# Kernel tuning notes

Hardware: AMD Instinct MI355X
Metric: run time of the kernel (lower is better)

The kernel has to match this reference:

```python
import jax, jax.numpy as jnp
import numpy as np

N_NODES = 100000
N_EDGES = 3200000
D_IN = 128
D_OUT = 128


def setup_inputs() -> dict:
    key = jax.random.key(0)
    kx, kw, kb, kr, kc, kv = jax.random.split(key, 6)
    x = jax.random.normal(kx, (N_NODES, D_IN), dtype=jnp.float32)
    W = jax.random.normal(kw, (D_OUT, D_IN), dtype=jnp.float32) * (1.0 / np.sqrt(D_IN))
    b = jax.random.normal(kb, (D_OUT,), dtype=jnp.float32) * 0.01
    adj_rows = jax.random.randint(kr, (N_EDGES,), 0, N_NODES, dtype=jnp.int32)
    adj_cols = jax.random.randint(kc, (N_EDGES,), 0, N_NODES, dtype=jnp.int32)
    adj_vals = jax.random.uniform(kv, (N_EDGES,), dtype=jnp.float32)
    return {"x": x, "W": W, "b": b, "adj_rows": adj_rows,
            "adj_cols": adj_cols, "adj_vals": adj_vals}


def reference(x, W, b, adj_rows, adj_cols, adj_vals):
    # linear: out = x @ W.T + b   -> [N, D_OUT]
    out = jnp.einsum('ni,oi->no', x, W) + b
    # spmm(adj, out): row r = sum over edges (r, c, v) of v * out[c]
    gathered = out[adj_cols] * adj_vals[:, None]          # [E, D_OUT]
    agg = jax.ops.segment_sum(gathered, adj_rows, num_segments=x.shape[0])
    return jax.nn.elu(agg)
```

## Files before the change

### kernel.cpp

```cpp
#include <hip/hip_runtime.h>
#include <hip/hip_bf16.h>
#include <cmath>

#define RPB      32
#define FB_CAP   1280
#define SB_SHIFT 11
#define NSB_MAX  64
#define TILE     2048
#define CH_PER_SB 34

typedef __attribute__((ext_vector_type(8))) short short8;
typedef __attribute__((ext_vector_type(4))) float floatx4;

__device__ __forceinline__ unsigned short f2bf(float f) {
    unsigned int u = __float_as_uint(f);
    u += 0x7FFFu + ((u >> 16) & 1u);
    return (unsigned short)(u >> 16);
}

__global__ __launch_bounds__(256) void gemm_mfma_kernel(
    const float* __restrict__ x, const float* __restrict__ W,
    const float* __restrict__ b, unsigned short* __restrict__ Yb, int N)
{
    __shared__ unsigned short Wb[128][136];
    __shared__ unsigned short Xb[64][136];
    const int t    = threadIdx.x;
    const int wave = t >> 6;
    const int lane = t & 63;
    const int col  = lane & 15;
    const int quad = lane >> 4;
    const int rowbase = blockIdx.x * 64;

#pragma unroll
    for (int i = 0; i < 16; ++i) {
        const int idx = t + 256 * i;
        const int o = idx >> 5, k4 = (idx & 31) * 4;
        const float4 v = *(const float4*)&W[(size_t)idx * 4];
        Wb[o][k4 + 0] = f2bf(v.x); Wb[o][k4 + 1] = f2bf(v.y);
        Wb[o][k4 + 2] = f2bf(v.z); Wb[o][k4 + 3] = f2bf(v.w);
    }
#pragma unroll
    for (int i = 0; i < 8; ++i) {
        const int idx = t + 256 * i;
        const int row = idx >> 5, k4 = (idx & 31) * 4;
        const int gr = rowbase + row;
        float4 v = make_float4(0.f, 0.f, 0.f, 0.f);
        if (gr < N) v = *(const float4*)&x[(size_t)gr * 128 + k4];
        Xb[row][k4 + 0] = f2bf(v.x); Xb[row][k4 + 1] = f2bf(v.y);
        Xb[row][k4 + 2] = f2bf(v.z); Xb[row][k4 + 3] = f2bf(v.w);
    }
    __syncthreads();

    float bias[8];
#pragma unroll
    for (int nt = 0; nt < 8; ++nt) bias[nt] = b[nt * 16 + col];

    floatx4 acc[8] = {};
    const int mrow = wave * 16;
#pragma unroll
    for (int k0 = 0; k0 < 128; k0 += 32) {
        const short8 a = *(const short8*)&Xb[mrow + col][k0 + quad * 8];
#pragma unroll
        for (int nt = 0; nt < 8; ++nt) {
            const short8 bf = *(const short8*)&Wb[nt * 16 + col][k0 + quad * 8];
            acc[nt] = __builtin_amdgcn_mfma_f32_16x16x32_bf16(a, bf, acc[nt], 0, 0, 0);
        }
    }
#pragma unroll
    for (int nt = 0; nt < 8; ++nt) {
#pragma unroll
        for (int reg = 0; reg < 4; ++reg) {
            const int gr = rowbase + mrow + quad * 4 + reg;
            if (gr < N)
                Yb[(size_t)gr * 128 + nt * 16 + col] = f2bf(acc[nt][reg] + bias[nt]);
        }
    }
}

__global__ __launch_bounds__(256) void init_cursor_kernel(
    int* __restrict__ cursor1, int* __restrict__ cursor2, int SB_CAP, int NB)
{
    const int i = blockIdx.x * blockDim.x + threadIdx.x;
    if (i < NSB_MAX) cursor1[i] = i * SB_CAP;
    if (i < NB)      cursor2[i] = i * FB_CAP;
}

__global__ __launch_bounds__(256) void pass1_kernel(
    const int* __restrict__ rows, const int* __restrict__ cols,
    const float* __restrict__ vals, int* __restrict__ cursor1,
    int2* __restrict__ pairs1, int E)
{
    __shared__ int2 sbuf[TILE];
    __shared__ unsigned char sbin[TILE];
    __shared__ unsigned short perm[TILE];
    __shared__ int hist[NSB_MAX], off[NSB_MAX], gbase[NSB_MAX], cur[NSB_MAX];
    const int t  = threadIdx.x;
    const int lane = t & 63;
    const int lo = blockIdx.x * TILE;
    const int cnt = min(TILE, E - lo);

    if (t < NSB_MAX) hist[t] = 0;
    __syncthreads();
    for (int i = t; i < cnt; i += 256) {
        const int   r = rows[lo + i];
        const int   c = cols[lo + i];
        const float v = vals[lo + i];
        sbuf[i] = make_int2(((r & 2047) << 17) | c, __float_as_int(v));
        const int bb = r >> SB_SHIFT;
        sbin[i] = (unsigned char)bb;
        atomicAdd(&hist[bb], 1);
    }
    __syncthreads();
    if (t < NSB_MAX) {
        const int h = hist[t];
        int s = h;
#pragma unroll
        for (int d = 1; d < NSB_MAX; d <<= 1) {
            const int n = __shfl_up(s, d);
            if (lane >= d) s += n;
        }
        off[t] = s - h;
        cur[t] = s - h;
        if (h > 0) gbase[t] = atomicAdd(&cursor1[t], h);
    }
    __syncthreads();
    for (int i = t; i < cnt; i += 256) {
        const int pos = atomicAdd(&cur[sbin[i]], 1);
        perm[pos] = (unsigned short)i;
    }
    __syncthreads();
    for (int i = t; i < cnt; i += 256) {
        const int src = perm[i];
        const int bb  = sbin[src];
        pairs1[gbase[bb] + (i - off[bb])] = sbuf[src];
    }
}

__global__ __launch_bounds__(256) void pass2_kernel(
    const int* __restrict__ cursor1, int* __restrict__ cursor2,
    const int2* __restrict__ pairs1, int2* __restrict__ pairs2, int SB_CAP)
{
    __shared__ int2 sbuf[TILE];
    __shared__ unsigned short perm[TILE];
    __shared__ int hist[64], off[64], gbase[64], cur[64];
    const int t   = threadIdx.x;
    const int lane = t & 63;
    const int sb  = blockIdx.x / CH_PER_SB;
    const int ch  = blockIdx.x % CH_PER_SB;
    const int base = sb * SB_CAP;
    const int scnt = cursor1[sb] - base;
    const int csz  = (scnt + CH_PER_SB - 1) / CH_PER_SB;
    const int lo   = ch * csz;
    const int cnt  = max(0, min(csz, scnt - lo));

    if (t < 64) hist[t] = 0;
    __syncthreads();
    for (int i = t; i < cnt; i += 256) {
        const int2 p = pairs1[base + lo + i];
        sbuf[i] = p;
        atomicAdd(&hist[(unsigned)p.x >> 22], 1);
    }
    __syncthreads();
    if (t < 64) {
        const int h = hist[t];
        int s = h;
#pragma unroll
        for (int d = 1; d < 64; d <<= 1) {
            const int n = __shfl_up(s, d);
            if (lane >= d) s += n;
        }
        off[t] = s - h;
        cur[t] = s - h;
        if (h > 0) gbase[t] = atomicAdd(&cursor2[sb * 64 + t], h);
    }
    __syncthreads();
    for (int i = t; i < cnt; i += 256) {
        const int pos = atomicAdd(&cur[(unsigned)sbuf[i].x >> 22], 1);
        perm[pos] = (unsigned short)i;
    }
    __syncthreads();
    for (int i = t; i < cnt; i += 256) {
        const int2 p = sbuf[perm[i]];
        const int bb = (unsigned)p.x >> 22;
        pairs2[gbase[bb] + (i - off[bb])] = make_int2(p.x & 0x3FFFFF, p.y);
    }
}

__global__ __launch_bounds__(256) void sortgather_kernel(
    const int* __restrict__ cursor2, const int2* __restrict__ pairs2,
    const unsigned int* __restrict__ Yu, float* __restrict__ out, int N)
{
    __shared__ __align__(16) int2 sbuf[FB_CAP];
    __shared__ __align__(16) int2 dbuf[FB_CAP + 8];
    __shared__ int hist[RPB];
    __shared__ int off[RPB];
    __shared__ int cur[RPB];
    const int b    = blockIdx.x;
    const int t    = threadIdx.x;
    const int w    = t >> 6;
    const int lane = t & 63;
    const int slot = b * FB_CAP;
    int cnt = cursor2[b] - slot;
    if (cnt > FB_CAP) cnt = FB_CAP;

    if (t < RPB) hist[t] = 0;
    __syncthreads();
    for (int i = t; i < cnt; i += 256) {
        const int2 p = pairs2[slot + i];
        sbuf[i] = p;
        atomicAdd(&hist[p.x >> 17], 1);
    }
    __syncthreads();
    if (t < RPB) {
        const int h = hist[t];
        int s = h;
#pragma unroll
        for (int d = 1; d < RPB; d <<= 1) {
            const int n = __shfl_up(s, d);
            if (lane >= d) s += n;
        }
        off[t] = s - h;
        cur[t] = s - h;
    }
    __syncthreads();
    for (int i = t; i < cnt; i += 256) {
        const int2 p   = sbuf[i];
        const int  pos = atomicAdd(&cur[p.x >> 17], 1);
        dbuf[pos] = make_int2(p.x & 0x1FFFF, p.y);
    }
    if (t < 8) dbuf[cnt + t] = make_int2(0, 0);
    __syncthreads();

    const int sub   = lane >> 4;
    const int qlane = lane & 15;

#pragma unroll
    for (int k = 0; k < RPB / 4; ++k) {
        const int rl = w * (RPB / 4) + k;
        const int gr = b * RPB + rl;
        const int s = off[rl];
        const int e = s + hist[rl];

        float acc0 = 0.f, acc1 = 0.f, acc2 = 0.f, acc3 = 0.f;
        float acc4 = 0.f, acc5 = 0.f, acc6 = 0.f, acc7 = 0.f;
#pragma unroll 2
        for (int j = s; j < e; j += 8) {
            const int2 pA = dbuf[j + sub];
            const int2 pB = dbuf[j + 4 + sub];
            float vA = __int_as_float(pA.y);
            float vB = __int_as_float(pB.y);
            vA = (j + sub < e)     ? vA : 0.0f;
            vB = (j + 4 + sub < e) ? vB : 0.0f;
            const uint4 yA = *(const uint4*)&Yu[((unsigned)pA.x << 6) + qlane * 4];
            const uint4 yB = *(const uint4*)&Yu[((unsigned)pB.x << 6) + qlane * 4];
            acc0 = fmaf(vA, __uint_as_float(yA.x << 16), acc0);
            acc1 = fmaf(vA, __uint_as_float(yA.x & 0xFFFF0000u), acc1);
            acc2 = fmaf(vA, __uint_as_float(yA.y << 16), acc2);
            acc3 = fmaf(vA, __uint_as_float(yA.y & 0xFFFF0000u), acc3);
            acc4 = fmaf(vA, __uint_as_float(yA.z << 16), acc4);
            acc5 = fmaf(vA, __uint_as_float(yA.z & 0xFFFF0000u), acc5);
            acc6 = fmaf(vA, __uint_as_float(yA.w << 16), acc6);
            acc7 = fmaf(vA, __uint_as_float(yA.w & 0xFFFF0000u), acc7);
            acc0 = fmaf(vB, __uint_as_float(yB.x << 16), acc0);
            acc1 = fmaf(vB, __uint_as_float(yB.x & 0xFFFF0000u), acc1);
            acc2 = fmaf(vB, __uint_as_float(yB.y << 16), acc2);
            acc3 = fmaf(vB, __uint_as_float(yB.y & 0xFFFF0000u), acc3);
            acc4 = fmaf(vB, __uint_as_float(yB.z << 16), acc4);
            acc5 = fmaf(vB, __uint_as_float(yB.z & 0xFFFF0000u), acc5);
            acc6 = fmaf(vB, __uint_as_float(yB.w << 16), acc6);
            acc7 = fmaf(vB, __uint_as_float(yB.w & 0xFFFF0000u), acc7);
        }
        acc0 += __shfl_xor(acc0, 32); acc1 += __shfl_xor(acc1, 32);
        acc2 += __shfl_xor(acc2, 32); acc3 += __shfl_xor(acc3, 32);
        acc4 += __shfl_xor(acc4, 32); acc5 += __shfl_xor(acc5, 32);
        acc6 += __shfl_xor(acc6, 32); acc7 += __shfl_xor(acc7, 32);
        acc0 += __shfl_xor(acc0, 16); acc1 += __shfl_xor(acc1, 16);
        acc2 += __shfl_xor(acc2, 16); acc3 += __shfl_xor(acc3, 16);
        acc4 += __shfl_xor(acc4, 16); acc5 += __shfl_xor(acc5, 16);
        acc6 += __shfl_xor(acc6, 16); acc7 += __shfl_xor(acc7, 16);

        if (lane < 16 && gr < N) {
            float4 o0, o1;
            o0.x = acc0 > 0.f ? acc0 : __expf(acc0) - 1.f;
            o0.y = acc1 > 0.f ? acc1 : __expf(acc1) - 1.f;
            o0.z = acc2 > 0.f ? acc2 : __expf(acc2) - 1.f;
            o0.w = acc3 > 0.f ? acc3 : __expf(acc3) - 1.f;
            o1.x = acc4 > 0.f ? acc4 : __expf(acc4) - 1.f;
            o1.y = acc5 > 0.f ? acc5 : __expf(acc5) - 1.f;
            o1.z = acc6 > 0.f ? acc6 : __expf(acc6) - 1.f;
            o1.w = acc7 > 0.f ? acc7 : __expf(acc7) - 1.f;
            float* po = &out[(size_t)gr * 128 + qlane * 8];
            *(float4*)po       = o0;
            *(float4*)(po + 4) = o1;
        }
    }
}

__global__ __launch_bounds__(256) void gemm_bias_kernel(
    const float* __restrict__ x, const float* __restrict__ W,
    const float* __restrict__ b, float* __restrict__ Y, int N)
{
    __shared__ float Wt[128][130];
    const int tid  = threadIdx.x;
    const int wave = tid >> 6;
    const int lane = tid & 63;
    for (int i = tid; i < 128 * 128; i += 256) {
        const int o = i >> 7, k = i & 127;
        Wt[k][o] = W[i];
    }
    __syncthreads();
    const float2 bv = *(const float2*)&b[2 * lane];
    for (int row = blockIdx.x * 4 + wave; row < N; row += gridDim.x * 4) {
        float acc0 = 0.f, acc1 = 0.f;
        for (int k = 0; k < 128; ++k) {
            const float2 w = *(const float2*)&Wt[k][2 * lane];
            const float xv = x[(size_t)row * 128 + k];
            acc0 = fmaf(xv, w.x, acc0);
            acc1 = fmaf(xv, w.y, acc1);
        }
        float2 o2; o2.x = acc0 + bv.x; o2.y = acc1 + bv.y;
        *(float2*)&Y[(size_t)row * 128 + 2 * lane] = o2;
    }
}

__global__ __launch_bounds__(256) void scatter_kernel(
    const int* __restrict__ rows, const int* __restrict__ cols,
    const float* __restrict__ vals, const float* __restrict__ Y,
    float* __restrict__ out, int E)
{
    const long long gid = (long long)blockIdx.x * blockDim.x + threadIdx.x;
    const int wid  = (int)(gid >> 6);
    const int lane = threadIdx.x & 63;
    if (wid >= E) return;
    const int   r = rows[wid];
    const int   c = cols[wid];
    const float v = vals[wid];
    const float2 y = *(const float2*)&Y[(size_t)c * 128 + 2 * lane];
    float* po = &out[(size_t)r * 128 + 2 * lane];
    atomicAdd(po,     v * y.x);
    atomicAdd(po + 1, v * y.y);
}

__global__ __launch_bounds__(256) void elu_kernel(float* __restrict__ out, int n4)
{
    int i = blockIdx.x * blockDim.x + threadIdx.x;
    const int stride = gridDim.x * blockDim.x;
    float4* p = (float4*)out;
    for (; i < n4; i += stride) {
        float4 v = p[i];
        v.x = v.x > 0.f ? v.x : expf(v.x) - 1.f;
        v.y = v.y > 0.f ? v.y : expf(v.y) - 1.f;
        v.z = v.z > 0.f ? v.z : expf(v.z) - 1.f;
        v.w = v.w > 0.f ? v.w : expf(v.w) - 1.f;
        p[i] = v;
    }
}

extern "C" void kernel_launch(void* const* d_in, const int* in_sizes, int n_in,
                              void* d_out, int out_size, void* d_ws, size_t ws_size,
                              hipStream_t stream)
{
    const float* x    = (const float*)d_in[0];
    const float* W    = (const float*)d_in[1];
    const float* b    = (const float*)d_in[2];
    const int*   rows = (const int*)d_in[3];
    const int*   cols = (const int*)d_in[4];
    const float* vals = (const float*)d_in[5];
    float* out = (float*)d_out;

    const int N   = in_sizes[0] / 128;
    const int E   = in_sizes[3];
    const int NB  = (N + RPB - 1) / RPB;
    const int NSB = (N + (1 << SB_SHIFT) - 1) >> SB_SHIFT;

    const int sb_mean = (E + NSB - 1) / NSB;
    int sbsig = 1; while (sbsig * sbsig < sb_mean) ++sbsig;
    const int SB_CAP = (sb_mean + 10 * sbsig + 63) & ~63;

    auto align256 = [](size_t v) { return (v + 255) & ~(size_t)255; };
    const size_t offPairs2 = 0;
    const size_t szPairs2  = (size_t)NB * FB_CAP * 8;
    const size_t offShared = align256(offPairs2 + szPairs2);
    const size_t szShared  = (size_t)NSB * SB_CAP * 8 > (size_t)N * 256
                           ? (size_t)NSB * SB_CAP * 8 : (size_t)N * 256;
    const size_t offCur1   = align256(offShared + szShared);
    const size_t offCur2   = align256(offCur1 + NSB_MAX * 4);
    const size_t need      = offCur2 + (size_t)NB * 4;

    const bool csr_ok = (need <= ws_size) && (NSB <= NSB_MAX) &&
                        ((long long)E <= (long long)NB * 1056) &&
                        (SB_CAP <= CH_PER_SB * TILE);

    if (csr_ok) {
        int2* pairs2        = (int2*)((char*)d_ws + offPairs2);
        int2* pairs1        = (int2*)((char*)d_ws + offShared);
        unsigned short* Yb  = (unsigned short*)((char*)d_ws + offShared);
        int*  cursor1       = (int*)((char*)d_ws + offCur1);
        int*  cursor2       = (int*)((char*)d_ws + offCur2);

        init_cursor_kernel<<<(NB + 255) / 256, 256, 0, stream>>>(cursor1, cursor2,
                                                                 SB_CAP, NB);
        pass1_kernel<<<(E + TILE - 1) / TILE, 256, 0, stream>>>(rows, cols, vals,
                                                                cursor1, pairs1, E);
        pass2_kernel<<<NSB * CH_PER_SB, 256, 0, stream>>>(cursor1, cursor2,
                                                          pairs1, pairs2, SB_CAP);
        gemm_mfma_kernel<<<(N + 63) / 64, 256, 0, stream>>>(x, W, b, Yb, N);
        sortgather_kernel<<<NB, 256, 0, stream>>>(cursor2, pairs2,
                                                  (const unsigned int*)Yb, out, N);
    } else {
        float* Y = (float*)d_ws;
        hipMemsetAsync(d_out, 0, (size_t)out_size * sizeof(float), stream);
        gemm_bias_kernel<<<512, 256, 0, stream>>>(x, W, b, Y, N);
        scatter_kernel<<<(E + 3) / 4, 256, 0, stream>>>(rows, cols, vals, Y, out, E);
        elu_kernel<<<1024, 256, 0, stream>>>(out, out_size / 4);
    }
}
```

Baseline: 312.5 us.

## Bin gathered edges by column slice so all rows sweep source nodes together

The sortgather kernel now buckets each block's edges by (column slice, row) into 256 bins. It then loops over slices in the outer loop, keeping eight row accumulators per wave in registers, so all waves gather from the same region of Y at roughly the same time. The intent is better L2/MALL locality for the random feature-row gathers. In exchange it uses many more registers (64 accumulator floats per lane), runs a two-level block scan, and gives up the 8-edge unrolled inner loop in favour of 4 edges per iteration, which lowers memory-level parallelism per row.

Result: slower. 345.0 us (+10.4%).

```diff
diff --git a/kernel.cpp b/kernel.cpp
--- a/kernel.cpp
+++ b/kernel.cpp
@@ -8,6 +8,8 @@
 #define NSB_MAX  64
 #define TILE     2048
 #define CH_PER_SB 34
+#define NSLICE   8
+#define BINS     (NSLICE * RPB)
 
 typedef __attribute__((ext_vector_type(8))) short short8;
 typedef __attribute__((ext_vector_type(4))) float floatx4;
@@ -192,9 +194,10 @@
 {
     __shared__ __align__(16) int2 sbuf[FB_CAP];
     __shared__ __align__(16) int2 dbuf[FB_CAP + 8];
-    __shared__ int hist[RPB];
-    __shared__ int off[RPB];
-    __shared__ int cur[RPB];
+    __shared__ int hist[BINS];
+    __shared__ int off[BINS];
+    __shared__ int cur[BINS];
+    __shared__ int csum[4];
     const int b    = blockIdx.x;
     const int t    = threadIdx.x;
     const int w    = t >> 6;
@@ -203,73 +206,78 @@
     int cnt = cursor2[b] - slot;
     if (cnt > FB_CAP) cnt = FB_CAP;
 
-    if (t < RPB) hist[t] = 0;
+    hist[t] = 0;
     __syncthreads();
     for (int i = t; i < cnt; i += 256) {
         const int2 p = pairs2[slot + i];
         sbuf[i] = p;
-        atomicAdd(&hist[p.x >> 17], 1);
-    }
-    __syncthreads();
-    if (t < RPB) {
+        const int bin = ((p.x & 0x1FFFF) >> 14) * RPB + (p.x >> 17);
+        atomicAdd(&hist[bin], 1);
+    }
+    __syncthreads();
+    {
         const int h = hist[t];
         int s = h;
 #pragma unroll
-        for (int d = 1; d < RPB; d <<= 1) {
+        for (int d = 1; d < 64; d <<= 1) {
             const int n = __shfl_up(s, d);
             if (lane >= d) s += n;
         }
-        off[t] = s - h;
-        cur[t] = s - h;
+        if (lane == 63) csum[w] = s;
+        __syncthreads();
+        int carry = 0;
+#pragma unroll
+        for (int k = 0; k < 3; ++k) carry += (k < w) ? csum[k] : 0;
+        off[t] = s - h + carry;
+        cur[t] = s - h + carry;
     }
     __syncthreads();
     for (int i = t; i < cnt; i += 256) {
         const int2 p   = sbuf[i];
-        const int  pos = atomicAdd(&cur[p.x >> 17], 1);
+        const int bin  = ((p.x & 0x1FFFF) >> 14) * RPB + (p.x >> 17);
+        const int pos  = atomicAdd(&cur[bin], 1);
         dbuf[pos] = make_int2(p.x & 0x1FFFF, p.y);
     }
-    if (t < 8) dbuf[cnt + t] = make_int2(0, 0);
     __syncthreads();
 
     const int sub   = lane >> 4;
     const int qlane = lane & 15;
 
-#pragma unroll
-    for (int k = 0; k < RPB / 4; ++k) {
-        const int rl = w * (RPB / 4) + k;
-        const int gr = b * RPB + rl;
-        const int s = off[rl];
-        const int e = s + hist[rl];
-
-        float acc0 = 0.f, acc1 = 0.f, acc2 = 0.f, acc3 = 0.f;
-        float acc4 = 0.f, acc5 = 0.f, acc6 = 0.f, acc7 = 0.f;
-#pragma unroll 2
-        for (int j = s; j < e; j += 8) {
-            const int2 pA = dbuf[j + sub];
-            const int2 pB = dbuf[j + 4 + sub];
-            float vA = __int_as_float(pA.y);
-            float vB = __int_as_float(pB.y);
-            vA = (j + sub < e)     ? vA : 0.0f;
-            vB = (j + 4 + sub < e) ? vB : 0.0f;
-            const uint4 yA = *(const uint4*)&Yu[((unsigned)pA.x << 6) + qlane * 4];
-            const uint4 yB = *(const uint4*)&Yu[((unsigned)pB.x << 6) + qlane * 4];
-            acc0 = fmaf(vA, __uint_as_float(yA.x << 16), acc0);
-            acc1 = fmaf(vA, __uint_as_float(yA.x & 0xFFFF0000u), acc1);
-            acc2 = fmaf(vA, __uint_as_float(yA.y << 16), acc2);
-            acc3 = fmaf(vA, __uint_as_float(yA.y & 0xFFFF0000u), acc3);
-            acc4 = fmaf(vA, __uint_as_float(yA.z << 16), acc4);
-            acc5 = fmaf(vA, __uint_as_float(yA.z & 0xFFFF0000u), acc5);
-            acc6 = fmaf(vA, __uint_as_float(yA.w << 16), acc6);
-            acc7 = fmaf(vA, __uint_as_float(yA.w & 0xFFFF0000u), acc7);
-            acc0 = fmaf(vB, __uint_as_float(yB.x << 16), acc0);
-            acc1 = fmaf(vB, __uint_as_float(yB.x & 0xFFFF0000u), acc1);
-            acc2 = fmaf(vB, __uint_as_float(yB.y << 16), acc2);
-            acc3 = fmaf(vB, __uint_as_float(yB.y & 0xFFFF0000u), acc3);
-            acc4 = fmaf(vB, __uint_as_float(yB.z << 16), acc4);
-            acc5 = fmaf(vB, __uint_as_float(yB.z & 0xFFFF0000u), acc5);
-            acc6 = fmaf(vB, __uint_as_float(yB.w << 16), acc6);
-            acc7 = fmaf(vB, __uint_as_float(yB.w & 0xFFFF0000u), acc7);
-        }
+    float4 aA[8], aB[8];
+#pragma unroll
+    for (int k = 0; k < 8; ++k) {
+        aA[k] = make_float4(0.f, 0.f, 0.f, 0.f);
+        aB[k] = make_float4(0.f, 0.f, 0.f, 0.f);
+    }
+
+    for (int s = 0; s < NSLICE; ++s) {
+#pragma unroll
+        for (int k = 0; k < 8; ++k) {
+            const int bin = s * RPB + w * 8 + k;
+            const int st  = off[bin];
+            const int e   = st + hist[bin];
+            for (int j = st; j < e; j += 4) {
+                const int2 p  = dbuf[j + sub];
+                const bool ok = (j + sub) < e;
+                const float v     = ok ? __int_as_float(p.y) : 0.0f;
+                const unsigned c  = ok ? (unsigned)p.x : 0u;
+                const uint4 y = *(const uint4*)&Yu[((size_t)c << 6) + qlane * 4];
+                aA[k].x = fmaf(v, __uint_as_float(y.x << 16), aA[k].x);
+                aA[k].y = fmaf(v, __uint_as_float(y.x & 0xFFFF0000u), aA[k].y);
+                aA[k].z = fmaf(v, __uint_as_float(y.y << 16), aA[k].z);
+                aA[k].w = fmaf(v, __uint_as_float(y.y & 0xFFFF0000u), aA[k].w);
+                aB[k].x = fmaf(v, __uint_as_float(y.z << 16), aB[k].x);
+                aB[k].y = fmaf(v, __uint_as_float(y.z & 0xFFFF0000u), aB[k].y);
+                aB[k].z = fmaf(v, __uint_as_float(y.w << 16), aB[k].z);
+                aB[k].w = fmaf(v, __uint_as_float(y.w & 0xFFFF0000u), aB[k].w);
+            }
+        }
+    }
+
+#pragma unroll
+    for (int k = 0; k < 8; ++k) {
+        float acc0 = aA[k].x, acc1 = aA[k].y, acc2 = aA[k].z, acc3 = aA[k].w;
+        float acc4 = aB[k].x, acc5 = aB[k].y, acc6 = aB[k].z, acc7 = aB[k].w;
         acc0 += __shfl_xor(acc0, 32); acc1 += __shfl_xor(acc1, 32);
         acc2 += __shfl_xor(acc2, 32); acc3 += __shfl_xor(acc3, 32);
         acc4 += __shfl_xor(acc4, 32); acc5 += __shfl_xor(acc5, 32);
@@ -279,6 +287,7 @@
         acc4 += __shfl_xor(acc4, 16); acc5 += __shfl_xor(acc5, 16);
         acc6 += __shfl_xor(acc6, 16); acc7 += __shfl_xor(acc7, 16);
 
+        const int gr = b * RPB + w * 8 + k;
         if (lane < 16 && gr < N) {
             float4 o0, o1;
             o0.x = acc0 > 0.f ? acc0 : __expf(acc0) - 1.f;
```
